# Kernel tuning notes

Measured on AMD Instinct MI355X. Metric: run time of the kernel, lower is better.

The kernel has to match this reference:

```python
import jax, jax.numpy as jnp
import numpy as np

# shift search range (matches init_kwargs)
MIN_SX, MAX_SX = -4, 4
MIN_SY, MAX_SY = -4, 4
B, C, H, W = 4, 3, 512, 512


def _shift(x, sx, sy):
    """torch.roll on dims (1,2) of a [C,H,W] tensor, zeroing wrapped rows/cols.

    Equivalent to AutomatedShiftFix.shift: positive sx zeros rows [:sx],
    negative sx zeros rows [sx:]; same for sy on the W axis.
    """
    h, w = x.shape[1], x.shape[2]
    shifted = jnp.roll(x, (sx, sy), axis=(1, 2))
    i = jnp.arange(h)[:, None]   # [H,1]
    j = jnp.arange(w)[None, :]   # [1,W]
    mask_h = jnp.where(sx >= 0, i >= sx, i < h + sx)
    mask_w = jnp.where(sy >= 0, j >= sy, j < w + sy)
    mask = (mask_h & mask_w).astype(x.dtype)  # [H,W]
    return shifted * mask[None]


def _all_shifts():
    sx = jnp.arange(MIN_SX, MAX_SX + 1)
    sy = jnp.arange(MIN_SY, MAX_SY + 1)
    # outer loop over shift_x, inner over shift_y -> 'ij' matches torch ordering
    return jnp.stack(jnp.meshgrid(sx, sy, indexing="ij"), axis=-1).reshape(-1, 2)  # [Ns,2]


def setup_inputs() -> dict:
    key = jax.random.key(0)
    k1, k2 = jax.random.split(key)
    x_ref = jax.random.normal(k1, (B, C, H, W), dtype=jnp.float32)
    x = jax.random.normal(k2, (B, C, H, W), dtype=jnp.float32)
    return {"x_ref": x_ref, "x": x}


def reference(x_ref, x):
    shifts = _all_shifts()  # [Ns,2] int32

    def sims_one(xr, xi):  # xr, xi: [C,H,W]
        # similarity for every candidate shift: sum over (C,H,W) of shifted*ref
        return jax.vmap(lambda s: jnp.sum(_shift(xi, s[0], s[1]) * xr))(shifts)  # [Ns]

    sims = jax.vmap(sims_one)(x_ref, x)          # [B, Ns]
    best = jnp.argmax(sims, axis=1)              # [B]
    best_shifts = shifts[best]                   # [B, 2]
    out = jax.vmap(lambda xi, s: _shift(xi, s[0], s[1]))(x, best_shifts)  # [B,C,H,W]
    return out, best_shifts
```

## Files before the change

kernel.cpp:

```cpp
#include <hip/hip_runtime.h>

#define BB 4
#define CC 3
#define HH 512
#define WW 512
#define NS 81
#define IMG (HH * WW)
#define CHW (CC * IMG)
#define STRIP 8
#define NSTRIPS (HH / STRIP)
#define NBLK (BB * NSTRIPS)
#define NROWS (CC * STRIP)

__device__ double g_part[NSTRIPS][BB * NS];
__device__ int    g_best[BB];

#define C4(v, i) ((i) == 0 ? (v).x : (i) == 1 ? (v).y : (i) == 2 ? (v).z : (v).w)

__global__ __launch_bounds__(576, 8) void k_sims(const float* __restrict__ xref,
                                                 const float* __restrict__ x) {
    int bid   = blockIdx.x;
    int strip = bid & (NSTRIPS - 1);
    int b     = bid >> 6;
    int tid  = threadIdx.x;
    int lane = tid & 63;
    int sxi  = tid >> 6;
    int j0   = lane << 3;
    int sx   = sxi - 4;
    int ip0  = strip * STRIP;

    const float* xbase = x    + (size_t)b * CHW;
    const float* rbase = xref + (size_t)b * CHW;

    float acc[9];
#pragma unroll
    for (int s = 0; s < 9; ++s) acc[s] = 0.f;

    float4 xa, xb, ra, rb, nxa, nxb, nra, nrb;
    bool okc;
    {
        int ii = ip0 + sx;
        okc = (unsigned)ii < HH;
        const float* xr = xbase + ip0 * WW + j0;
        const float* rr_ = rbase + (okc ? ii : ip0) * WW + j0;
        xa = *(const float4*)xr;   xb = *(const float4*)(xr + 4);
        ra = *(const float4*)rr_;  rb = *(const float4*)(rr_ + 4);
    }

#pragma unroll 2
    for (int t = 0; t < NROWS; ++t) {
        bool okn = false;
        if (t < NROWS - 1) {
            int tn = t + 1;
            int c  = tn >> 3;
            int ip = ip0 + (tn & 7);
            int ii = ip + sx;
            okn = (unsigned)ii < HH;
            const float* xr  = xbase + (size_t)c * IMG + ip * WW + j0;
            const float* rr_ = rbase + (size_t)c * IMG + (okn ? ii : ip) * WW + j0;
            nxa = *(const float4*)xr;   nxb = *(const float4*)(xr + 4);
            nra = *(const float4*)rr_;  nrb = *(const float4*)(rr_ + 4);
        }

        if (okc) {
            float p0 = __shfl_up(rb.x, 1, 64);
            float p1 = __shfl_up(rb.y, 1, 64);
            float p2 = __shfl_up(rb.z, 1, 64);
            float p3 = __shfl_up(rb.w, 1, 64);
            if (lane == 0) { p0 = p1 = p2 = p3 = 0.f; }
            float n0 = __shfl_down(ra.x, 1, 64);
            float n1 = __shfl_down(ra.y, 1, 64);
            float n2 = __shfl_down(ra.z, 1, 64);
            float n3 = __shfl_down(ra.w, 1, 64);
            if (lane == 63) { n0 = n1 = n2 = n3 = 0.f; }

#define P4(i) ((i) == 0 ? p0 : (i) == 1 ? p1 : (i) == 2 ? p2 : p3)
#define N4(i) ((i) == 0 ? n0 : (i) == 1 ? n1 : (i) == 2 ? n2 : n3)
#pragma unroll
            for (int syi = 0; syi < 9; ++syi) {
#pragma unroll
                for (int k = 0; k < 8; ++k) {
                    int i = k + syi;
                    float wv = (i < 4)  ? P4(i)
                             : (i < 8)  ? C4(ra, i - 4)
                             : (i < 12) ? C4(rb, i - 8)
                             :            N4(i - 12);
                    float xv = (k < 4) ? C4(xa, k) : C4(xb, k - 4);
                    acc[syi] += xv * wv;
                }
            }
#undef P4
#undef N4
        }

        xa = nxa; xb = nxb; ra = nra; rb = nrb; okc = okn;
    }

#pragma unroll
    for (int s = 0; s < 9; ++s) {
        float v = acc[s];
        for (int off = 32; off; off >>= 1) v += __shfl_down(v, off, 64);
        if (lane == 0)
            g_part[strip][b * NS + sxi * 9 + s] = (double)v;
    }
}

__global__ __launch_bounds__(384) void k_reduce(float* __restrict__ outTail) {
    int t = threadIdx.x;
    __shared__ double vals[BB * NS];
    if (t < BB * NS) {
        double s = 0.0;
#pragma unroll 4
        for (int k = 0; k < NSTRIPS; ++k) s += g_part[k][t];
        vals[t] = s;
    }
    __syncthreads();
    if (t < BB) {
        const double* v = vals + t * NS;
        int best = 0;
        double bv = v[0];
        for (int i = 1; i < NS; ++i)
            if (v[i] > bv) { bv = v[i]; best = i; }
        g_best[t] = best;
        outTail[t * 2]     = (float)(best / 9 - 4);
        outTail[t * 2 + 1] = (float)(best % 9 - 4);
    }
}

__global__ __launch_bounds__(256) void k_apply(const float* __restrict__ x,
                                               float* __restrict__ out) {
    int blk = blockIdx.x;
    int bc  = blk >> 8;
    int tid = threadIdx.x;
    int b   = bc / CC;

    int bi = g_best[b];
    int sx = bi / 9 - 4;
    int sy = bi % 9 - 4;

    int row = ((blk & 255) << 1) + (tid >> 7);
    int j0  = (tid & 127) << 2;
    int is  = row - sx;
    float4 v = make_float4(0.f, 0.f, 0.f, 0.f);
    if ((unsigned)is < HH) {
        const float* src = x + (size_t)bc * IMG + is * WW;
        int js0 = j0 - sy;
        if (js0 >= 0 && js0 + 3 < WW) {
            v = *(const float4*)(src + js0);
        } else {
            float* vv = (float*)&v;
#pragma unroll
            for (int k = 0; k < 4; ++k) {
                int js = js0 + k;
                if ((unsigned)js < WW) vv[k] = src[js];
            }
        }
    }
    *(float4*)(out + (size_t)bc * IMG + row * WW + j0) = v;
}

extern "C" void kernel_launch(void* const* d_in, const int* in_sizes, int n_in,
                              void* d_out, int out_size, void* d_ws, size_t ws_size,
                              hipStream_t stream) {
    const float* xref = (const float*)d_in[0];
    const float* x    = (const float*)d_in[1];
    float* out = (float*)d_out;
    (void)d_ws; (void)ws_size;

    k_sims<<<NBLK, 576, 0, stream>>>(xref, x);
    k_reduce<<<1, 384, 0, stream>>>(out + (size_t)BB * CHW);

    int applyBlocks = (BB * CC * HH) / 2;
    k_apply<<<applyBlocks, 256, 0, stream>>>(x, out);
}
```

Measured before the change: 96.54 us.

## Fuse sims, reduce and apply into one cooperative kernel with grid sync

Merges the similarity, argmax-reduce and shift-apply kernels into a single cooperative launch with a grid-wide sync. Each block redundantly reduces the partial sums to find the best shifts, then applies the shift to its share of rows. This removes two kernel launches and the global best-index round trip. In exchange the apply phase runs on only 256 blocks and every block repeats the reduction, which may reduce memory parallelism.

```diff
diff --git a/kernel.cpp b/kernel.cpp
--- a/kernel.cpp
+++ b/kernel.cpp
@@ -1,4 +1,7 @@
 #include <hip/hip_runtime.h>
+#include <hip/hip_cooperative_groups.h>
+
+namespace cg = cooperative_groups;
 
 #define BB 4
 #define CC 3
@@ -11,14 +14,16 @@
 #define NSTRIPS (HH / STRIP)
 #define NBLK (BB * NSTRIPS)
 #define NROWS (CC * STRIP)
+#define ROWS_PER_BLK ((BB * CC * HH) / NBLK)
 
 __device__ double g_part[NSTRIPS][BB * NS];
-__device__ int    g_best[BB];
 
 #define C4(v, i) ((i) == 0 ? (v).x : (i) == 1 ? (v).y : (i) == 2 ? (v).z : (v).w)
 
-__global__ __launch_bounds__(576, 8) void k_sims(const float* __restrict__ xref,
-                                                 const float* __restrict__ x) {
+__global__ __launch_bounds__(576, 8) void k_all(const float* __restrict__ xref,
+                                                const float* __restrict__ x,
+                                                float* __restrict__ out,
+                                                float* __restrict__ outTail) {
     int bid   = blockIdx.x;
     int strip = bid & (NSTRIPS - 1);
     int b     = bid >> 6;
@@ -41,7 +46,7 @@
     {
         int ii = ip0 + sx;
         okc = (unsigned)ii < HH;
-        const float* xr = xbase + ip0 * WW + j0;
+        const float* xr  = xbase + ip0 * WW + j0;
         const float* rr_ = rbase + (okc ? ii : ip0) * WW + j0;
         xa = *(const float4*)xr;   xb = *(const float4*)(xr + 4);
         ra = *(const float4*)rr_;  rb = *(const float4*)(rr_ + 4);
@@ -103,60 +108,61 @@
         if (lane == 0)
             g_part[strip][b * NS + sxi * 9 + s] = (double)v;
     }
-}
 
-__global__ __launch_bounds__(384) void k_reduce(float* __restrict__ outTail) {
-    int t = threadIdx.x;
+    cg::this_grid().sync();
+
     __shared__ double vals[BB * NS];
-    if (t < BB * NS) {
+    __shared__ int    sBest[BB];
+    if (tid < BB * NS) {
         double s = 0.0;
 #pragma unroll 4
-        for (int k = 0; k < NSTRIPS; ++k) s += g_part[k][t];
-        vals[t] = s;
+        for (int k = 0; k < NSTRIPS; ++k) s += g_part[k][tid];
+        vals[tid] = s;
     }
     __syncthreads();
-    if (t < BB) {
-        const double* v = vals + t * NS;
+    if (tid < BB) {
+        const double* v = vals + tid * NS;
         int best = 0;
         double bv = v[0];
         for (int i = 1; i < NS; ++i)
             if (v[i] > bv) { bv = v[i]; best = i; }
-        g_best[t] = best;
-        outTail[t * 2]     = (float)(best / 9 - 4);
-        outTail[t * 2 + 1] = (float)(best % 9 - 4);
+        sBest[tid] = best;
+        if (bid == 0) {
+            outTail[tid * 2]     = (float)(best / 9 - 4);
+            outTail[tid * 2 + 1] = (float)(best % 9 - 4);
+        }
     }
-}
+    __syncthreads();
 
-__global__ __launch_bounds__(256) void k_apply(const float* __restrict__ x,
-                                               float* __restrict__ out) {
-    int blk = blockIdx.x;
-    int bc  = blk >> 8;
-    int tid = threadIdx.x;
-    int b   = bc / CC;
-
-    int bi = g_best[b];
-    int sx = bi / 9 - 4;
-    int sy = bi % 9 - 4;
-
-    int row = ((blk & 255) << 1) + (tid >> 7);
-    int j0  = (tid & 127) << 2;
-    int is  = row - sx;
-    float4 v = make_float4(0.f, 0.f, 0.f, 0.f);
-    if ((unsigned)is < HH) {
-        const float* src = x + (size_t)bc * IMG + is * WW;
-        int js0 = j0 - sy;
-        if (js0 >= 0 && js0 + 3 < WW) {
-            v = *(const float4*)(src + js0);
-        } else {
-            float* vv = (float*)&v;
+    for (int idx = tid; idx < ROWS_PER_BLK * (WW / 4); idx += 576) {
+        int rloc = idx >> 7;
+        int jf4  = idx & 127;
+        int grow = bid * ROWS_PER_BLK + rloc;
+        int bc   = grow >> 9;
+        int row  = grow & 511;
+        int bb   = bc / CC;
+        int bi = sBest[bb];
+        int psx = bi / 9 - 4;
+        int psy = bi % 9 - 4;
+        int is  = row - psx;
+        int jc  = jf4 << 2;
+        float4 v = make_float4(0.f, 0.f, 0.f, 0.f);
+        if ((unsigned)is < HH) {
+            const float* src = x + (size_t)bc * IMG + is * WW;
+            int js0 = jc - psy;
+            if (js0 >= 0 && js0 + 3 < WW) {
+                v = *(const float4*)(src + js0);
+            } else {
+                float* vv = (float*)&v;
 #pragma unroll
-            for (int k = 0; k < 4; ++k) {
-                int js = js0 + k;
-                if ((unsigned)js < WW) vv[k] = src[js];
+                for (int k = 0; k < 4; ++k) {
+                    int js = js0 + k;
+                    if ((unsigned)js < WW) vv[k] = src[js];
+                }
             }
         }
+        *(float4*)(out + (size_t)bc * IMG + row * WW + jc) = v;
     }
-    *(float4*)(out + (size_t)bc * IMG + row * WW + j0) = v;
 }
 
 extern "C" void kernel_launch(void* const* d_in, const int* in_sizes, int n_in,
@@ -164,12 +170,11 @@
                               hipStream_t stream) {
     const float* xref = (const float*)d_in[0];
     const float* x    = (const float*)d_in[1];
-    float* out = (float*)d_out;
+    float* out     = (float*)d_out;
+    float* outTail = out + (size_t)BB * CHW;
     (void)d_ws; (void)ws_size;
 
-    k_sims<<<NBLK, 576, 0, stream>>>(xref, x);
-    k_reduce<<<1, 384, 0, stream>>>(out + (size_t)BB * CHW);
-
-    int applyBlocks = (BB * CC * HH) / 2;
-    k_apply<<<applyBlocks, 256, 0, stream>>>(x, out);
+    void* args[] = { (void*)&xref, (void*)&x, (void*)&out, (void*)&outTail };
+    hipLaunchCooperativeKernel((const void*)k_all, dim3(NBLK), dim3(576),
+                               args, 0, stream);
 }
```

After: 133.6 us. 1.38x slower.
